# Kernel optimization log

Measured on AMD Instinct MI355X. Metric: run time of the kernel, lower is better.

Reference implementation:

```python
import jax, jax.numpy as jnp
import numpy as np
import math

C = 512
D = C // 4  # 128
SCALE = math.sqrt(D)

def setup_inputs() -> dict:
    key = jax.random.key(0)
    k1, k2, k3, k4 = jax.random.split(key, 4)
    x = jax.random.normal(k1, (8, C, 2048), dtype=jnp.float32)
    # q_conv and k_conv share the same weight (tied in the torch module)
    wqk = jax.random.normal(k2, (D, C), dtype=jnp.float32) * (1.0 / math.sqrt(C))
    wv = jax.random.normal(k3, (D, C), dtype=jnp.float32) * (1.0 / math.sqrt(C))
    bv = jax.random.normal(k4, (D,), dtype=jnp.float32) * 0.01
    return {"x": x, "wqk": wqk, "wv": wv, "bv": bv}

def reference(x, wqk, wv, bv):
    # x: [B, C, N]; 1x1 conv == matmul over channel dim
    xq = jnp.einsum('dc,bcn->bnd', wqk, x)          # [B, N, D]
    xk = jnp.einsum('dc,bcn->bdn', wqk, x)          # [B, D, N]
    xv = jnp.einsum('dc,bcn->bdn', wv, x) + bv[None, :, None]  # [B, D, N]
    energy = jnp.einsum('bnd,bdm->bnm', xq, xk) / SCALE  # [B, N, N]
    attention = jax.nn.softmax(energy, axis=-1)
    x_r = jnp.einsum('bdn,bnm->bdm', xv, attention)  # [B, D, N]
    return x_r
```

## Files before the change

kernel.cpp:

```cpp
#include <hip/hip_runtime.h>

typedef short short4v __attribute__((ext_vector_type(4)));
typedef short short8 __attribute__((ext_vector_type(8)));
typedef float floatx4 __attribute__((ext_vector_type(4)));
typedef unsigned int uint;
typedef unsigned short ushort;

#define CH 512
#define NN 2048
#define DD 128
#define RSCALE 0.08838834764831845f

__device__ __forceinline__ float bf2f(ushort u) {
    union { uint i; float f; } v; v.i = ((uint)u) << 16; return v.f;
}
__device__ __forceinline__ ushort f2bf(float f) {
    union { float f; uint u; } v; v.f = f;
    uint u = v.u;
    return (ushort)((u + 0x7fffu + ((u >> 16) & 1u)) >> 16);
}

__global__ __launch_bounds__(256) void k0_prep(
    const float* __restrict__ wqk, const float* __restrict__ wv,
    ushort* __restrict__ Wbf, float* __restrict__ lsum,
    float* __restrict__ out)
{
    int gid = blockIdx.x * 256 + threadIdx.x;
    if (gid < 32768) {
        int base = gid * 4;
        const float* src = (base < 65536) ? (wqk + base) : (wv + base - 65536);
        float4 v = *(const float4*)src;
        short4v o;
        o[0] = (short)f2bf(v.x); o[1] = (short)f2bf(v.y);
        o[2] = (short)f2bf(v.z); o[3] = (short)f2bf(v.w);
        *(short4v*)&Wbf[base] = o;
    }
    if (gid < 16384) lsum[gid] = 0.0f;
    float4 z; z.x = 0.f; z.y = 0.f; z.z = 0.f; z.w = 0.f;
#pragma unroll
    for (int i = 0; i < 4; i++)
        *(float4*)&out[(size_t)(gid + i * 131072) * 4] = z;
}

__global__ __launch_bounds__(256) void k1_proj(
    const float* __restrict__ x,
    const ushort* __restrict__ Wbf,
    const float* __restrict__ bv,
    ushort* __restrict__ Q,
    ushort* __restrict__ VT)
{
    const int nt = blockIdx.x;
    const int h  = blockIdx.y;
    const int b  = blockIdx.z;
    const int n0 = nt * 32;
    const int t = threadIdx.x;
    const int lane = t & 63, w = t >> 6, l15 = lane & 15, quad = lane >> 4;

    __shared__ __attribute__((aligned(16))) ushort As[32 * 72];
    __shared__ __attribute__((aligned(16))) ushort Bs[128 * 72];
    __shared__ __attribute__((aligned(16))) ushort Vt[128 * 40];

    floatx4 acc[2][2];
#pragma unroll
    for (int i = 0; i < 2; i++)
#pragma unroll
        for (int j = 0; j < 2; j++) acc[i][j] = (floatx4)(0.0f);

    const float* xb = x + b * (CH * NN) + n0;
    const ushort* Wh = Wbf + h * 128 * CH;

    const int an = t & 31, ag = t >> 5;

    for (int c0 = 0; c0 < CH; c0 += 64) {
        {
            short8 v;
#pragma unroll
            for (int i = 0; i < 8; i++)
                v[i] = (short)f2bf(xb[(c0 + ag * 8 + i) * NN + an]);
            *(short8*)&As[an * 72 + ag * 8] = v;
        }
#pragma unroll
        for (int rep = 0; rep < 4; rep++) {
            int idx = rep * 256 + t;
            int row = idx >> 3, g = idx & 7;
            *(short8*)&Bs[row * 72 + g * 8] = *(const short8*)&Wh[row * CH + c0 + g * 8];
        }
        __syncthreads();
#pragma unroll
        for (int kd = 0; kd < 2; kd++) {
            short8 a0 = *(short8*)&As[(l15) * 72 + kd * 32 + quad * 8];
            short8 a1 = *(short8*)&As[(16 + l15) * 72 + kd * 32 + quad * 8];
#pragma unroll
            for (int dt2 = 0; dt2 < 2; dt2++) {
                short8 bf = *(short8*)&Bs[(w * 32 + dt2 * 16 + l15) * 72 + kd * 32 + quad * 8];
                acc[0][dt2] = __builtin_amdgcn_mfma_f32_16x16x32_bf16(a0, bf, acc[0][dt2], 0, 0, 0);
                acc[1][dt2] = __builtin_amdgcn_mfma_f32_16x16x32_bf16(a1, bf, acc[1][dt2], 0, 0, 0);
            }
        }
        __syncthreads();
    }

#pragma unroll
    for (int ns = 0; ns < 2; ns++)
#pragma unroll
        for (int dt2 = 0; dt2 < 2; dt2++) {
            int ds_ = w * 32 + dt2 * 16 + l15;
#pragma unroll
            for (int r = 0; r < 4; r++) {
                int nl = ns * 16 + quad * 4 + r;
                float val = acc[ns][dt2][r];
                if (h == 0) {
                    Q[b * (NN * DD) + (n0 + nl) * DD + ds_] = f2bf(val);
                } else {
                    Vt[ds_ * 40 + nl] = f2bf(val + bv[ds_]);
                }
            }
        }
    if (h == 1) {
        __syncthreads();
#pragma unroll
        for (int rep = 0; rep < 2; rep++) {
            int idx = rep * 256 + t;
            int dv = idx >> 2, seg = idx & 3;
            *(short8*)&VT[((size_t)b * DD + dv) * NN + n0 + seg * 8] =
                *(short8*)&Vt[dv * 40 + seg * 8];
        }
    }
}

__global__ __launch_bounds__(256, 4) void k_p(
    const ushort* __restrict__ Q,
    ushort* __restrict__ P,
    float* __restrict__ lsum)
{
    const int pid = blockIdx.x;
    const int b = blockIdx.y;
    const int it = pid >> 4, jt = pid & 15;
    const int i0 = it * 128, j0 = jt * 128;
    const int t = threadIdx.x;
    const int lane = t & 63, w = t >> 6, l15 = lane & 15, quad = lane >> 4;
    const int wi = (w >> 1) * 64, wj = (w & 1) * 64;

    __shared__ __attribute__((aligned(16))) char smem[36864];
    ushort* Qi = (ushort*)smem;
    ushort* Qj = (ushort*)(smem + 18432);
    ushort* Pt = (ushort*)smem;

    const ushort* Qb = Q + b * (NN * DD);

    floatx4 acc[4][4];
#pragma unroll
    for (int i = 0; i < 4; i++)
#pragma unroll
        for (int j = 0; j < 4; j++) acc[i][j] = (floatx4)(0.0f);

    for (int kh = 0; kh < 2; kh++) {
        if (kh) __syncthreads();
#pragma unroll
        for (int rep = 0; rep < 4; rep++) {
            int idx = rep * 256 + t;
            int row = idx >> 3, g = idx & 7;
            *(short8*)&Qi[row * 72 + g * 8] = *(const short8*)&Qb[(i0 + row) * DD + kh * 64 + g * 8];
            *(short8*)&Qj[row * 72 + g * 8] = *(const short8*)&Qb[(j0 + row) * DD + kh * 64 + g * 8];
        }
        __syncthreads();

#pragma unroll
        for (int kd = 0; kd < 2; kd++) {
            short8 afr[4], bfr[4];
#pragma unroll
            for (int nt = 0; nt < 4; nt++)
                afr[nt] = *(short8*)&Qi[(wi + nt * 16 + l15) * 72 + kd * 32 + quad * 8];
#pragma unroll
            for (int mt = 0; mt < 4; mt++)
                bfr[mt] = *(short8*)&Qj[(wj + mt * 16 + l15) * 72 + kd * 32 + quad * 8];
#pragma unroll
            for (int nt = 0; nt < 4; nt++)
#pragma unroll
                for (int mt = 0; mt < 4; mt++)
                    acc[nt][mt] = __builtin_amdgcn_mfma_f32_16x16x32_bf16(afr[nt], bfr[mt], acc[nt][mt], 0, 0, 0);
        }
    }

    __syncthreads();

#pragma unroll
    for (int nt = 0; nt < 4; nt++) {
        float rs[4] = {0.f, 0.f, 0.f, 0.f};
#pragma unroll
        for (int mt = 0; mt < 4; mt++)
#pragma unroll
            for (int r = 0; r < 4; r++) {
                float p = __expf(acc[nt][mt][r] * RSCALE);
                rs[r] += p;
                Pt[(wi + nt * 16 + quad * 4 + r) * 138 + wj + mt * 16 + l15] = f2bf(p);
            }
#pragma unroll
        for (int r = 0; r < 4; r++) {
            float s = rs[r];
            s += __shfl_xor(s, 1);
            s += __shfl_xor(s, 2);
            s += __shfl_xor(s, 4);
            s += __shfl_xor(s, 8);
            if (l15 == 0)
                atomicAdd(&lsum[b * NN + i0 + wi + nt * 16 + quad * 4 + r], s);
        }
    }
    __syncthreads();

    ushort* Pb = P + (size_t)b * NN * NN;
#pragma unroll
    for (int rep = 0; rep < 8; rep++) {
        int idx = rep * 256 + t;
        int row = idx >> 4, g = idx & 15;
        *(short8*)&Pb[(size_t)(i0 + row) * NN + j0 + g * 8] =
            *(short8*)&Pt[row * 138 + g * 8];
    }
}

__global__ __launch_bounds__(256) void k_vscale(
    const ushort* __restrict__ VT, const float* __restrict__ lsum,
    ushort* __restrict__ Vsc)
{
    int gid = blockIdx.x * 256 + threadIdx.x;
    size_t idx = (size_t)gid * 8;
    int b = (int)(idx >> 18);
    int n = (int)(idx & (NN - 1));
    short8 v = *(const short8*)&VT[idx];
    float4 l0 = *(const float4*)&lsum[b * NN + n];
    float4 l1 = *(const float4*)&lsum[b * NN + n + 4];
    short8 o;
    o[0] = (short)f2bf(bf2f((ushort)v[0]) / l0.x);
    o[1] = (short)f2bf(bf2f((ushort)v[1]) / l0.y);
    o[2] = (short)f2bf(bf2f((ushort)v[2]) / l0.z);
    o[3] = (short)f2bf(bf2f((ushort)v[3]) / l0.w);
    o[4] = (short)f2bf(bf2f((ushort)v[4]) / l1.x);
    o[5] = (short)f2bf(bf2f((ushort)v[5]) / l1.y);
    o[6] = (short)f2bf(bf2f((ushort)v[6]) / l1.z);
    o[7] = (short)f2bf(bf2f((ushort)v[7]) / l1.w);
    *(short8*)&Vsc[idx] = o;
}

__global__ __launch_bounds__(256, 4) void k_pv(
    const ushort* __restrict__ Vsc,
    const ushort* __restrict__ P,
    float* __restrict__ out)
{
    const int mt = blockIdx.x;
    const int h  = blockIdx.y;
    const int b  = blockIdx.z;
    const int m0 = mt * 32;
    const int t = threadIdx.x;
    const int lane = t & 63, w = t >> 6, l15 = lane & 15, quad = lane >> 4;

    __shared__ __attribute__((aligned(16))) ushort Vs[128 * 72];
    __shared__ __attribute__((aligned(16))) ushort Pp[32 * 72];

    const ushort* Vb = Vsc + (size_t)b * DD * NN;
    const ushort* Pb = P + (size_t)b * NN * NN;

    floatx4 acc[2][2];
#pragma unroll
    for (int i = 0; i < 2; i++)
#pragma unroll
        for (int j = 0; j < 2; j++) acc[i][j] = (floatx4)(0.0f);

    const int vsd = t >> 3, vsg = t & 7;
    const int psr = t >> 3, psg = t & 7;

    short8 vr[4], pr;

#define LOADR(NC)                                                              \
    do {                                                                       \
        _Pragma("unroll")                                                      \
        for (int rep = 0; rep < 4; rep++)                                      \
            vr[rep] = *(const short8*)&Vb[(size_t)(rep * 32 + vsd) * NN + (NC) + vsg * 8]; \
        pr = *(const short8*)&Pb[(size_t)(m0 + psr) * NN + (NC) + psg * 8];    \
    } while (0)

    const int nbeg = h * (NN / 2), nend = nbeg + (NN / 2);

    LOADR(nbeg);

    for (int n0c = nbeg; n0c < nend; n0c += 64) {
        __syncthreads();
#pragma unroll
        for (int rep = 0; rep < 4; rep++)
            *(short8*)&Vs[(rep * 32 + vsd) * 72 + vsg * 8] = vr[rep];
        *(short8*)&Pp[psr * 72 + psg * 8] = pr;
        __syncthreads();

        if (n0c + 64 < nend) LOADR(n0c + 64);

#pragma unroll
        for (int kn = 0; kn < 2; kn++) {
            short8 va0 = *(short8*)&Vs[(w * 32 + l15) * 72 + kn * 32 + quad * 8];
            short8 va1 = *(short8*)&Vs[(w * 32 + 16 + l15) * 72 + kn * 32 + quad * 8];
#pragma unroll
            for (int mf = 0; mf < 2; mf++) {
                short8 pb = *(short8*)&Pp[(mf * 16 + l15) * 72 + kn * 32 + quad * 8];
                acc[0][mf] = __builtin_amdgcn_mfma_f32_16x16x32_bf16(va0, pb, acc[0][mf], 0, 0, 0);
                acc[1][mf] = __builtin_amdgcn_mfma_f32_16x16x32_bf16(va1, pb, acc[1][mf], 0, 0, 0);
            }
        }
    }
#undef LOADR

    float* ob = out + (size_t)b * DD * NN;
#pragma unroll
    for (int dsub = 0; dsub < 2; dsub++)
#pragma unroll
        for (int mf = 0; mf < 2; mf++)
#pragma unroll
            for (int r = 0; r < 4; r++) {
                int d = w * 32 + dsub * 16 + quad * 4 + r;
                atomicAdd(&ob[(size_t)d * NN + m0 + mf * 16 + l15], acc[dsub][mf][r]);
            }
}

__global__ __launch_bounds__(256, 4) void kl_sum(
    const ushort* __restrict__ Q,
    float* __restrict__ lsum)
{
    int pid = blockIdx.x;
    const int b = blockIdx.y;
    int it = 0;
    while (pid >= (16 - it)) { pid -= (16 - it); it++; }
    const int jt = it + pid;
    const int i0 = it * 128, j0 = jt * 128;
    const int t = threadIdx.x;
    const int lane = t & 63, w = t >> 6, l15 = lane & 15, quad = lane >> 4;
    const int wi = (w >> 1) * 64, wj = (w & 1) * 64;

    __shared__ __attribute__((aligned(16))) ushort Qi[128 * 72];
    __shared__ __attribute__((aligned(16))) ushort Qj[128 * 72];

    const ushort* Qb = Q + b * (NN * DD);

    floatx4 acc[4][4];
#pragma unroll
    for (int i = 0; i < 4; i++)
#pragma unroll
        for (int j = 0; j < 4; j++) acc[i][j] = (floatx4)(0.0f);

    for (int kh = 0; kh < 2; kh++) {
        if (kh) __syncthreads();
#pragma unroll
        for (int rep = 0; rep < 4; rep++) {
            int idx = rep * 256 + t;
            int row = idx >> 3, g = idx & 7;
            *(short8*)&Qi[row * 72 + g * 8] = *(const short8*)&Qb[(i0 + row) * DD + kh * 64 + g * 8];
            *(short8*)&Qj[row * 72 + g * 8] = *(const short8*)&Qb[(j0 + row) * DD + kh * 64 + g * 8];
        }
        __syncthreads();

#pragma unroll
        for (int kd = 0; kd < 2; kd++) {
            short8 afr[4], bfr[4];
#pragma unroll
            for (int nt = 0; nt < 4; nt++)
                afr[nt] = *(short8*)&Qi[(wi + nt * 16 + l15) * 72 + kd * 32 + quad * 8];
#pragma unroll
            for (int mt = 0; mt < 4; mt++)
                bfr[mt] = *(short8*)&Qj[(wj + mt * 16 + l15) * 72 + kd * 32 + quad * 8];
#pragma unroll
            for (int nt = 0; nt < 4; nt++)
#pragma unroll
                for (int mt = 0; mt < 4; mt++)
                    acc[nt][mt] = __builtin_amdgcn_mfma_f32_16x16x32_bf16(afr[nt], bfr[mt], acc[nt][mt], 0, 0, 0);
        }
    }

    float cs[4] = {0.f, 0.f, 0.f, 0.f};
#pragma unroll
    for (int nt = 0; nt < 4; nt++) {
        float rs[4] = {0.f, 0.f, 0.f, 0.f};
#pragma unroll
        for (int mt = 0; mt < 4; mt++)
#pragma unroll
            for (int r = 0; r < 4; r++) {
                float p = __expf(acc[nt][mt][r] * RSCALE);
                rs[r] += p;
                cs[mt] += p;
            }
#pragma unroll
        for (int r = 0; r < 4; r++) {
            float s = rs[r];
            s += __shfl_xor(s, 1);
            s += __shfl_xor(s, 2);
            s += __shfl_xor(s, 4);
            s += __shfl_xor(s, 8);
            if (l15 == 0)
                atomicAdd(&lsum[b * NN + i0 + wi + nt * 16 + quad * 4 + r], s);
        }
    }
    if (it != jt) {
#pragma unroll
        for (int mt = 0; mt < 4; mt++) {
            float s = cs[mt];
            s += __shfl_xor(s, 16);
            s += __shfl_xor(s, 32);
            if (lane < 16)
                atomicAdd(&lsum[b * NN + j0 + wj + mt * 16 + l15], s);
        }
    }
}

__global__ __launch_bounds__(256, 4) void k_fused_sep(
    const ushort* __restrict__ Q,
    const ushort* __restrict__ VT,
    const float* __restrict__ lsum,
    float* __restrict__ out)
{
    const int mt = blockIdx.x;
    const int h  = blockIdx.y;
    const int b  = blockIdx.z;
    const int m0 = mt * 32;
    const int t = threadIdx.x;
    const int lane = t & 63, w = t >> 6, l15 = lane & 15, quad = lane >> 4;

    __shared__ __attribute__((aligned(16))) ushort Qn[64 * 136];
    __shared__ __attribute__((aligned(16))) ushort Vs[128 * 72];
    __shared__ __attribute__((aligned(16))) ushort Ps[32 * 68];

    const ushort* Qb = Q + b * (NN * DD);
    const ushort* VTb = VT + (size_t)b * DD * NN;
    const float* lb = lsum + b * NN;

#pragma unroll
    for (int rep = 0; rep < 2; rep++) {
        int idx = rep * 256 + t;
        int row = idx >> 4, g = idx & 15;
        *(short8*)&Qn[row * 136 + g * 8] = *(const short8*)&Qb[(m0 + row) * DD + g * 8];
    }
    __syncthreads();

    short8 qm[2][4];
#pragma unroll
    for (int ms = 0; ms < 2; ms++)
#pragma unroll
        for (int kd = 0; kd < 4; kd++)
            qm[ms][kd] = *(short8*)&Qn[(ms * 16 + l15) * 136 + kd * 32 + quad * 8];

    floatx4 acc[2][2];
#pragma unroll
    for (int i = 0; i < 2; i++)
#pragma unroll
        for (int j = 0; j < 2; j++) acc[i][j] = (floatx4)(0.0f);

    const int qsr = t >> 4, qsg = t & 15;
    const int vsd = t >> 3, vsg = t & 7;

    short8 qr[4], vr[4];

#define LOADR(NC)                                                              \
    do {                                                                       \
        _Pragma("unroll")                                                      \
        for (int rep = 0; rep < 4; rep++)                                      \
            qr[rep] = *(const short8*)&Qb[((NC) + rep * 16 + qsr) * DD + qsg * 8]; \
        _Pragma("unroll")                                                      \
        for (int rep = 0; rep < 4; rep++)                                      \
            vr[rep] = *(const short8*)&VTb[(size_t)(rep * 32 + vsd) * NN + (NC) + vsg * 8]; \
    } while (0)

    const int nbeg = h * (NN / 2), nend = nbeg + (NN / 2);

    LOADR(nbeg);

    for (int n0c = nbeg; n0c < nend; n0c += 64) {
        float lw = lb[n0c + w * 16 + l15];
        __syncthreads();
#pragma unroll
        for (int rep = 0; rep < 4; rep++)
            *(short8*)&Qn[(rep * 16 + qsr) * 136 + qsg * 8] = qr[rep];
#pragma unroll
        for (int rep = 0; rep < 4; rep++)
            *(short8*)&Vs[(rep * 32 + vsd) * 72 + vsg * 8] = vr[rep];
        __syncthreads();

        if (n0c + 64 < nend) LOADR(n0c + 64);

        {
            float linv = 1.0f / lw;
            short8 bq[4];
#pragma unroll
            for (int kd = 0; kd < 4; kd++)
                bq[kd] = *(short8*)&Qn[(w * 16 + l15) * 136 + kd * 32 + quad * 8];
#pragma unroll
            for (int ms = 0; ms < 2; ms++) {
                floatx4 s = (floatx4)(0.0f);
#pragma unroll
                for (int kd = 0; kd < 4; kd++)
                    s = __builtin_amdgcn_mfma_f32_16x16x32_bf16(qm[ms][kd], bq[kd], s, 0, 0, 0);
#pragma unroll
                for (int r = 0; r < 4; r++) {
                    float p = __expf(s[r] * RSCALE) * linv;
                    Ps[(ms * 16 + quad * 4 + r) * 68 + w * 16 + l15] = f2bf(p);
                }
            }
        }
        __syncthreads();

#pragma unroll
        for (int kn = 0; kn < 2; kn++) {
            short8 va0 = *(short8*)&Vs[(w * 32 + l15) * 72 + kn * 32 + quad * 8];
            short8 va1 = *(short8*)&Vs[(w * 32 + 16 + l15) * 72 + kn * 32 + quad * 8];
#pragma unroll
            for (int mf = 0; mf < 2; mf++) {
                short8 pb = *(short8*)&Ps[(mf * 16 + l15) * 68 + kn * 32 + quad * 8];
                acc[0][mf] = __builtin_amdgcn_mfma_f32_16x16x32_bf16(va0, pb, acc[0][mf], 0, 0, 0);
                acc[1][mf] = __builtin_amdgcn_mfma_f32_16x16x32_bf16(va1, pb, acc[1][mf], 0, 0, 0);
            }
        }
    }
#undef LOADR

    float* ob = out + (size_t)b * DD * NN;
#pragma unroll
    for (int dsub = 0; dsub < 2; dsub++)
#pragma unroll
        for (int mf = 0; mf < 2; mf++)
#pragma unroll
            for (int r = 0; r < 4; r++) {
                int d = w * 32 + dsub * 16 + quad * 4 + r;
                atomicAdd(&ob[(size_t)d * NN + m0 + mf * 16 + l15], acc[dsub][mf][r]);
            }
}

__global__ __launch_bounds__(256) void k1_fb(
    const float* __restrict__ x, const float* __restrict__ wqk,
    const float* __restrict__ wv, const float* __restrict__ bv,
    ushort* __restrict__ Q, ushort* __restrict__ V)
{
    const int nt = blockIdx.x;
    const int b  = blockIdx.y;
    const int n0 = nt * 32;
    const int t = threadIdx.x;
    const int lane = t & 63, w = t >> 6, l15 = lane & 15, quad = lane >> 4;

    __shared__ __attribute__((aligned(16))) ushort As[32 * 40];
    __shared__ __attribute__((aligned(16))) ushort Bs[256 * 40];

    floatx4 acc[2][4];
#pragma unroll
    for (int i = 0; i < 2; i++)
#pragma unroll
        for (int j = 0; j < 4; j++) acc[i][j] = (floatx4)(0.0f);

    const float* xb = x + b * (CH * NN) + n0;

    for (int c0 = 0; c0 < CH; c0 += 32) {
        {
            int n = t & 31, g = t >> 5;
            short4v v;
#pragma unroll
            for (int i = 0; i < 4; i++)
                v[i] = (short)f2bf(xb[(c0 + g * 4 + i) * NN + n]);
            *(short4v*)&As[n * 40 + g * 4] = v;
        }
#pragma unroll
        for (int rep = 0; rep < 16; rep++) {
            int idx = rep * 256 + t;
            int row = idx >> 4, cp = idx & 15;
            const float* wf = (row < 128) ? (wqk + row * CH) : (wv + (row - 128) * CH);
            uint pack = (uint)f2bf(wf[c0 + cp * 2]) | ((uint)f2bf(wf[c0 + cp * 2 + 1]) << 16);
            *(uint*)&Bs[row * 40 + cp * 2] = pack;
        }
        __syncthreads();
        short8 a0 = *(short8*)&As[(l15) * 40 + quad * 8];
        short8 a1 = *(short8*)&As[(16 + l15) * 40 + quad * 8];
#pragma unroll
        for (int dt2 = 0; dt2 < 4; dt2++) {
            short8 bf = *(short8*)&Bs[(w * 64 + dt2 * 16 + l15) * 40 + quad * 8];
            acc[0][dt2] = __builtin_amdgcn_mfma_f32_16x16x32_bf16(a0, bf, acc[0][dt2], 0, 0, 0);
            acc[1][dt2] = __builtin_amdgcn_mfma_f32_16x16x32_bf16(a1, bf, acc[1][dt2], 0, 0, 0);
        }
        __syncthreads();
    }
#pragma unroll
    for (int ns = 0; ns < 2; ns++)
#pragma unroll
        for (int dt2 = 0; dt2 < 4; dt2++) {
            int ds_ = w * 64 + dt2 * 16 + l15;
#pragma unroll
            for (int r = 0; r < 4; r++) {
                int n = n0 + ns * 16 + quad * 4 + r;
                float val = acc[ns][dt2][r];
                if (ds_ < 128) {
                    Q[b * (NN * DD) + n * DD + ds_] = f2bf(val);
                } else {
                    int dv = ds_ - 128;
                    V[b * (NN * DD) + n * DD + dv] = f2bf(val + bv[dv]);
                }
            }
        }
}

__global__ __launch_bounds__(256) void k2_norm(
    const ushort* __restrict__ Q, ushort* __restrict__ V)
{
    const int ntile = blockIdx.x;
    const int b = blockIdx.y;
    const int n0 = ntile * 64;
    const int t = threadIdx.x;
    const int lane = t & 63, w = t >> 6, l15 = lane & 15, quad = lane >> 4;

    __shared__ __attribute__((aligned(16))) ushort Qs[64 * 136];
    __shared__ __attribute__((aligned(16))) ushort Qm2[64 * 136];

    const ushort* Qb = Q + b * (NN * DD);

#pragma unroll
    for (int rep = 0; rep < 16; rep++) {
        int idx = rep * 256 + t;
        int row = idx >> 6, dp = idx & 63;
        *(uint*)&Qs[row * 136 + dp * 2] = *(const uint*)&Qb[(n0 + row) * DD + dp * 2];
    }
    __syncthreads();

    short8 afr[4];
#pragma unroll
    for (int kd = 0; kd < 4; kd++)
        afr[kd] = *(short8*)&Qs[(w * 16 + l15) * 136 + kd * 32 + quad * 8];

    float sums[4] = {0.f, 0.f, 0.f, 0.f};

    for (int m0 = 0; m0 < NN; m0 += 64) {
#pragma unroll
        for (int rep = 0; rep < 16; rep++) {
            int idx = rep * 256 + t;
            int row = idx >> 6, dp = idx & 63;
            *(uint*)&Qm2[row * 136 + dp * 2] = *(const uint*)&Qb[(m0 + row) * DD + dp * 2];
        }
        __syncthreads();
#pragma unroll
        for (int ct = 0; ct < 4; ct++) {
            floatx4 s = (floatx4)(0.0f);
#pragma unroll
            for (int kd = 0; kd < 4; kd++) {
                short8 bf = *(short8*)&Qm2[(ct * 16 + l15) * 136 + kd * 32 + quad * 8];
                s = __builtin_amdgcn_mfma_f32_16x16x32_bf16(afr[kd], bf, s, 0, 0, 0);
            }
#pragma unroll
            for (int r = 0; r < 4; r++)
                sums[r] += __expf(s[r] * RSCALE);
        }
        __syncthreads();
    }

#pragma unroll
    for (int r = 0; r < 4; r++) {
        float s = sums[r];
        s += __shfl_xor(s, 1);
        s += __shfl_xor(s, 2);
        s += __shfl_xor(s, 4);
        s += __shfl_xor(s, 8);
        sums[r] = s;
    }

    ushort* Vb = V + b * (NN * DD);
#pragma unroll
    for (int r = 0; r < 4; r++) {
        int n = n0 + w * 16 + quad * 4 + r;
        float inv = 1.0f / sums[r];
        short8 vv = *(short8*)&Vb[n * DD + l15 * 8];
        short8 o;
#pragma unroll
        for (int i = 0; i < 8; i++)
            o[i] = (short)f2bf(bf2f((ushort)vv[i]) * inv);
        *(short8*)&Vb[n * DD + l15 * 8] = o;
    }
}

__global__ __launch_bounds__(256) void k3_attn(
    const ushort* __restrict__ Q, const ushort* __restrict__ Vp,
    float* __restrict__ out)
{
    const int mtile = blockIdx.x;
    const int b = blockIdx.y;
    const int m0 = mtile * 64;
    const int t = threadIdx.x;
    const int lane = t & 63, w = t >> 6, l15 = lane & 15, quad = lane >> 4;

    __shared__ __attribute__((aligned(16))) ushort Qs[64 * 136];
    __shared__ __attribute__((aligned(16))) ushort Qn2[32 * 136];
    __shared__ __attribute__((aligned(16))) ushort Vs2[128 * 40];
    __shared__ __attribute__((aligned(16))) ushort Ps2[64 * 40];

    const ushort* Qb = Q + b * (NN * DD);
    const ushort* Vpb = Vp + b * (NN * DD);

#pragma unroll
    for (int rep = 0; rep < 16; rep++) {
        int idx = rep * 256 + t;
        int row = idx >> 6, dp = idx & 63;
        *(uint*)&Qs[row * 136 + dp * 2] = *(const uint*)&Qb[(m0 + row) * DD + dp * 2];
    }
    __syncthreads();

    short8 afr[4];
#pragma unroll
    for (int kd = 0; kd < 4; kd++)
        afr[kd] = *(short8*)&Qs[(w * 16 + l15) * 136 + kd * 32 + quad * 8];

    floatx4 acc[2][4];
#pragma unroll
    for (int s = 0; s < 2; s++)
#pragma unroll
        for (int mt = 0; mt < 4; mt++) acc[s][mt] = (floatx4)(0.0f);

    for (int n0c = 0; n0c < NN; n0c += 32) {
#pragma unroll
        for (int rep = 0; rep < 8; rep++) {
            int idx = rep * 256 + t;
            int row = idx >> 6, dp = idx & 63;
            *(uint*)&Qn2[row * 136 + dp * 2] = *(const uint*)&Qb[(n0c + row) * DD + dp * 2];
        }
#pragma unroll
        for (int rep = 0; rep < 8; rep++) {
            int idx = rep * 256 + t;
            int np = idx >> 7, d = idx & 127;
            uint v0 = Vpb[(n0c + np * 2) * DD + d];
            uint v1 = Vpb[(n0c + np * 2 + 1) * DD + d];
            *(uint*)&Vs2[d * 40 + np * 2] = v0 | (v1 << 16);
        }
        __syncthreads();

#pragma unroll
        for (int nt2 = 0; nt2 < 2; nt2++) {
            floatx4 s = (floatx4)(0.0f);
#pragma unroll
            for (int kd = 0; kd < 4; kd++) {
                short8 bf = *(short8*)&Qn2[(nt2 * 16 + l15) * 136 + kd * 32 + quad * 8];
                s = __builtin_amdgcn_mfma_f32_16x16x32_bf16(afr[kd], bf, s, 0, 0, 0);
            }
#pragma unroll
            for (int r = 0; r < 4; r++) {
                float p = __expf(s[r] * RSCALE);
                Ps2[(w * 16 + quad * 4 + r) * 40 + nt2 * 16 + l15] = f2bf(p);
            }
        }
        __syncthreads();

        short8 pb[4];
#pragma unroll
        for (int mt = 0; mt < 4; mt++)
            pb[mt] = *(short8*)&Ps2[(mt * 16 + l15) * 40 + quad * 8];
#pragma unroll
        for (int sub = 0; sub < 2; sub++) {
            short8 va = *(short8*)&Vs2[(w * 32 + sub * 16 + l15) * 40 + quad * 8];
#pragma unroll
            for (int mt = 0; mt < 4; mt++)
                acc[sub][mt] = __builtin_amdgcn_mfma_f32_16x16x32_bf16(va, pb[mt], acc[sub][mt], 0, 0, 0);
        }
        __syncthreads();
    }

    float* ob = out + (size_t)b * DD * NN;
#pragma unroll
    for (int sub = 0; sub < 2; sub++)
#pragma unroll
        for (int mt = 0; mt < 4; mt++)
#pragma unroll
            for (int r = 0; r < 4; r++) {
                int d = w * 32 + sub * 16 + quad * 4 + r;
                int m = m0 + mt * 16 + l15;
                ob[(size_t)d * NN + m] = acc[sub][mt][r];
            }
}

extern "C" void kernel_launch(void* const* d_in, const int* in_sizes, int n_in,
                              void* d_out, int out_size, void* d_ws, size_t ws_size,
                              hipStream_t stream) {
    const float* x   = (const float*)d_in[0];
    const float* wqk = (const float*)d_in[1];
    const float* wv  = (const float*)d_in[2];
    const float* bv  = (const float*)d_in[3];
    float* out = (float*)d_out;

    ushort* Q = (ushort*)d_ws;

    if (ws_size >= ((size_t)80 << 20)) {
        ushort* VT   = (ushort*)((char*)d_ws + (4u << 20));
        ushort* Wbf  = (ushort*)((char*)d_ws + (8u << 20));
        float*  lsum = (float*)((char*)d_ws + (8u << 20) + (256u << 10));
        ushort* Vsc  = (ushort*)((char*)d_ws + (9u << 20));
        ushort* P    = (ushort*)((char*)d_ws + (16u << 20));

        k0_prep<<<512, 256, 0, stream>>>(wqk, wv, Wbf, lsum, out);
        k1_proj<<<dim3(64, 2, 8), 256, 0, stream>>>(x, Wbf, bv, Q, VT);
        k_p<<<dim3(256, 8), 256, 0, stream>>>(Q, P, lsum);
        k_vscale<<<1024, 256, 0, stream>>>(VT, lsum, Vsc);
        k_pv<<<dim3(64, 2, 8), 256, 0, stream>>>(Vsc, P, out);
    } else if (ws_size >= (size_t)33 * 1024 * 1024) {
        ushort* VT   = (ushort*)((char*)d_ws + (4u << 20));
        ushort* Wbf  = (ushort*)((char*)d_ws + (8u << 20));
        float*  lsum = (float*)((char*)d_ws + (8u << 20) + (256u << 10));

        k0_prep<<<512, 256, 0, stream>>>(wqk, wv, Wbf, lsum, out);
        k1_proj<<<dim3(64, 2, 8), 256, 0, stream>>>(x, Wbf, bv, Q, VT);
        kl_sum<<<dim3(136, 8), 256, 0, stream>>>(Q, lsum);
        k_fused_sep<<<dim3(64, 2, 8), 256, 0, stream>>>(Q, VT, lsum, out);
    } else {
        ushort* V = (ushort*)((char*)d_ws + (4u << 20));
        k1_fb<<<dim3(64, 8), 256, 0, stream>>>(x, wqk, wv, bv, Q, V);
        k2_norm<<<dim3(32, 8), 256, 0, stream>>>(Q, V);
        k3_attn<<<dim3(32, 8), 256, 0, stream>>>(Q, V, out);
    }
}
```

Baseline: 149.7 us.

## Exploit energy symmetry in P kernel and drop split-K atomics in PV

Because Q and K share weights, the energy matrix is symmetric. The P kernel now computes only the upper-triangular 128x128 tiles (136 blocks instead of 256). For each off-diagonal tile it also writes the transposed exp tile and adds column sums into lsum. The PV kernel no longer splits N across two blocks, so it writes output with plain stores instead of atomics. This halves the QQ^T matmul work but adds a second exp pass and an extra shared-memory transpose per off-diagonal tile, and PV has half as many blocks.

```diff
diff --git a/kernel.cpp b/kernel.cpp
--- a/kernel.cpp
+++ b/kernel.cpp
@@ -133,9 +133,11 @@
     ushort* __restrict__ P,
     float* __restrict__ lsum)
 {
-    const int pid = blockIdx.x;
+    int pid = blockIdx.x;
     const int b = blockIdx.y;
-    const int it = pid >> 4, jt = pid & 15;
+    int it = 0;
+    while (pid >= (16 - it)) { pid -= (16 - it); it++; }
+    const int jt = it + pid;
     const int i0 = it * 128, j0 = jt * 128;
     const int t = threadIdx.x;
     const int lane = t & 63, w = t >> 6, l15 = lane & 15, quad = lane >> 4;
@@ -184,6 +186,7 @@
 
     __syncthreads();
 
+    float cs[4] = {0.f, 0.f, 0.f, 0.f};
 #pragma unroll
     for (int nt = 0; nt < 4; nt++) {
         float rs[4] = {0.f, 0.f, 0.f, 0.f};
@@ -193,6 +196,7 @@
             for (int r = 0; r < 4; r++) {
                 float p = __expf(acc[nt][mt][r] * RSCALE);
                 rs[r] += p;
+                cs[mt] += p;
                 Pt[(wi + nt * 16 + quad * 4 + r) * 138 + wj + mt * 16 + l15] = f2bf(p);
             }
 #pragma unroll
@@ -206,6 +210,16 @@
                 atomicAdd(&lsum[b * NN + i0 + wi + nt * 16 + quad * 4 + r], s);
         }
     }
+    if (it != jt) {
+#pragma unroll
+        for (int mt = 0; mt < 4; mt++) {
+            float s = cs[mt];
+            s += __shfl_xor(s, 16);
+            s += __shfl_xor(s, 32);
+            if (lane < 16)
+                atomicAdd(&lsum[b * NN + j0 + wj + mt * 16 + l15], s);
+        }
+    }
     __syncthreads();
 
     ushort* Pb = P + (size_t)b * NN * NN;
@@ -215,6 +229,27 @@
         int row = idx >> 4, g = idx & 15;
         *(short8*)&Pb[(size_t)(i0 + row) * NN + j0 + g * 8] =
             *(short8*)&Pt[row * 138 + g * 8];
+    }
+
+    if (it != jt) {
+        __syncthreads();
+#pragma unroll
+        for (int nt = 0; nt < 4; nt++)
+#pragma unroll
+            for (int mt = 0; mt < 4; mt++)
+#pragma unroll
+                for (int r = 0; r < 4; r++) {
+                    float p = __expf(acc[nt][mt][r] * RSCALE);
+                    Pt[(wj + mt * 16 + l15) * 138 + wi + nt * 16 + quad * 4 + r] = f2bf(p);
+                }
+        __syncthreads();
+#pragma unroll
+        for (int rep = 0; rep < 8; rep++) {
+            int idx = rep * 256 + t;
+            int row = idx >> 4, g = idx & 15;
+            *(short8*)&Pb[(size_t)(j0 + row) * NN + i0 + g * 8] =
+                *(short8*)&Pt[row * 138 + g * 8];
+        }
     }
 }
 
@@ -247,8 +282,7 @@
     float* __restrict__ out)
 {
     const int mt = blockIdx.x;
-    const int h  = blockIdx.y;
-    const int b  = blockIdx.z;
+    const int b  = blockIdx.y;
     const int m0 = mt * 32;
     const int t = threadIdx.x;
     const int lane = t & 63, w = t >> 6, l15 = lane & 15, quad = lane >> 4;
@@ -278,11 +312,9 @@
         pr = *(const short8*)&Pb[(size_t)(m0 + psr) * NN + (NC) + psg * 8];    \
     } while (0)
 
-    const int nbeg = h * (NN / 2), nend = nbeg + (NN / 2);
-
-    LOADR(nbeg);
-
-    for (int n0c = nbeg; n0c < nend; n0c += 64) {
+    LOADR(0);
+
+    for (int n0c = 0; n0c < NN; n0c += 64) {
         __syncthreads();
 #pragma unroll
         for (int rep = 0; rep < 4; rep++)
@@ -290,7 +322,7 @@
         *(short8*)&Pp[psr * 72 + psg * 8] = pr;
         __syncthreads();
 
-        if (n0c + 64 < nend) LOADR(n0c + 64);
+        if (n0c + 64 < NN) LOADR(n0c + 64);
 
 #pragma unroll
         for (int kn = 0; kn < 2; kn++) {
@@ -314,7 +346,7 @@
 #pragma unroll
             for (int r = 0; r < 4; r++) {
                 int d = w * 32 + dsub * 16 + quad * 4 + r;
-                atomicAdd(&ob[(size_t)d * NN + m0 + mf * 16 + l15], acc[dsub][mf][r]);
+                ob[(size_t)d * NN + m0 + mf * 16 + l15] = acc[dsub][mf][r];
             }
 }
 
@@ -789,9 +821,9 @@
 
         k0_prep<<<512, 256, 0, stream>>>(wqk, wv, Wbf, lsum, out);
         k1_proj<<<dim3(64, 2, 8), 256, 0, stream>>>(x, Wbf, bv, Q, VT);
-        k_p<<<dim3(256, 8), 256, 0, stream>>>(Q, P, lsum);
+        k_p<<<dim3(136, 8), 256, 0, stream>>>(Q, P, lsum);
         k_vscale<<<1024, 256, 0, stream>>>(VT, lsum, Vsc);
-        k_pv<<<dim3(64, 2, 8), 256, 0, stream>>>(Vsc, P, out);
+        k_pv<<<dim3(64, 8), 256, 0, stream>>>(Vsc, P, out);
     } else if (ws_size >= (size_t)33 * 1024 * 1024) {
         ushort* VT   = (ushort*)((char*)d_ws + (4u << 20));
         ushort* Wbf  = (ushort*)((char*)d_ws + (8u << 20));
```

Measured after the change: 149.9 us. Within noise of the previous version (+0.1%).
